# Optimization experiments

Measured on AMD Instinct MI355X. Metric: run time of the kernel, lower is better.

The kernel has to match this reference:

```python
import jax, jax.numpy as jnp
import numpy as np

N, IN_DIM, OUT_DIM = 8192, 256, 64
NEG_INF = -9e15
SLOPE = 0.2


def setup_inputs() -> dict:
    key = jax.random.key(0)
    k1, k2, k3, k4 = jax.random.split(key, 4)
    h = jax.random.normal(k1, (N, IN_DIM), dtype=jnp.float32)
    adj = jax.random.randint(k2, (N, N), 0, 2, dtype=jnp.int32)
    W = jax.random.normal(k3, (IN_DIM, OUT_DIM), dtype=jnp.float32) * (1.0 / np.sqrt(IN_DIM))
    a = jax.random.normal(k4, (2 * OUT_DIM,), dtype=jnp.float32) * (1.0 / np.sqrt(2 * OUT_DIM))
    return {"h": h, "adj": adj, "W": W, "a": a}


def reference(h, adj, W, a):
    # Wh: [N, F]
    Wh = h @ W
    F = Wh.shape[-1]
    # a([Wh_i ; Wh_j]) decomposes: score_ij = a_left.Wh_i + a_right.Wh_j
    f_i = Wh @ a[:F]          # [N]
    f_j = Wh @ a[F:]          # [N]
    e = f_i[:, None] + f_j[None, :]            # [N, N] broadcast sum
    e = jnp.where(e >= 0, e, SLOPE * e)         # leaky relu (0.2)
    e = jnp.where(adj > 0, e, jnp.float32(NEG_INF))
    alpha = jax.nn.softmax(e, axis=1)           # row softmax over neighbors j
    return alpha @ Wh                            # [N, F]
```

## Files before the change

### kernel.cpp

```cpp
#include <hip/hip_runtime.h>

#define NN 8192
#define KDIM 256
#define FDIM 64
#define SLOPEC 0.2f

typedef __attribute__((ext_vector_type(8))) short bf16x8;
typedef __attribute__((ext_vector_type(4))) float f32x4;

__device__ __forceinline__ unsigned short f2bf(float x) {
    union { float f; unsigned u; } v; v.f = x;
    unsigned r = v.u + 0x7FFFu + ((v.u >> 16) & 1u);
    return (unsigned short)(r >> 16);
}

__device__ __forceinline__ float wred64(float v) {
    v += __shfl_xor(v, 1);
    v += __shfl_xor(v, 2);
    v += __shfl_xor(v, 4);
    v += __shfl_xor(v, 8);
    v += __shfl_xor(v, 16);
    v += __shfl_xor(v, 32);
    return v;
}

__global__ __launch_bounds__(256) void gat_phase1(
    const float* __restrict__ h, const float* __restrict__ W,
    const float* __restrict__ a, unsigned short* __restrict__ wfrag,
    float* __restrict__ fi, float* __restrict__ fj)
{
    __shared__ unsigned short wht_s[FDIM][20];
    const int tid = threadIdx.x;
    const int f  = tid & 63;
    const int rg = tid >> 6;
    const int i0 = blockIdx.x << 4;

    const float* __restrict__ h0 = h + (size_t)(i0 + rg * 4) * KDIM;
    const float* __restrict__ h1 = h0 + KDIM;
    const float* __restrict__ h2 = h0 + 2 * KDIM;
    const float* __restrict__ h3 = h0 + 3 * KDIM;

    float acc0 = 0.f, acc1 = 0.f, acc2 = 0.f, acc3 = 0.f;
    #pragma unroll 4
    for (int k4 = 0; k4 < KDIM / 4; ++k4) {
        const float4 r0 = *(const float4*)(h0 + k4 * 4);
        const float4 r1 = *(const float4*)(h1 + k4 * 4);
        const float4 r2 = *(const float4*)(h2 + k4 * 4);
        const float4 r3 = *(const float4*)(h3 + k4 * 4);
        const float w0 = W[(k4 * 4 + 0) * FDIM + f];
        const float w1 = W[(k4 * 4 + 1) * FDIM + f];
        const float w2 = W[(k4 * 4 + 2) * FDIM + f];
        const float w3 = W[(k4 * 4 + 3) * FDIM + f];
        acc0 += r0.x * w0 + r0.y * w1 + r0.z * w2 + r0.w * w3;
        acc1 += r1.x * w0 + r1.y * w1 + r1.z * w2 + r1.w * w3;
        acc2 += r2.x * w0 + r2.y * w1 + r2.z * w2 + r2.w * w3;
        acc3 += r3.x * w0 + r3.y * w1 + r3.z * w2 + r3.w * w3;
    }

    const int r0i = rg * 4;
    wht_s[f][r0i + 0] = f2bf(acc0);
    wht_s[f][r0i + 1] = f2bf(acc1);
    wht_s[f][r0i + 2] = f2bf(acc2);
    wht_s[f][r0i + 3] = f2bf(acc3);

    const float aL = a[f];
    const float aR = a[FDIM + f];
    float s;
    s = wred64(acc0 * aL); if (f == 0) fi[i0 + r0i + 0] = s;
    s = wred64(acc1 * aL); if (f == 0) fi[i0 + r0i + 1] = s;
    s = wred64(acc2 * aL); if (f == 0) fi[i0 + r0i + 2] = s;
    s = wred64(acc3 * aL); if (f == 0) fi[i0 + r0i + 3] = s;
    s = wred64(acc0 * aR); if (f == 0) fj[i0 + r0i + 0] = s;
    s = wred64(acc1 * aR); if (f == 0) fj[i0 + r0i + 1] = s;
    s = wred64(acc2 * aR); if (f == 0) fj[i0 + r0i + 2] = s;
    s = wred64(acc3 * aR); if (f == 0) fj[i0 + r0i + 3] = s;

    __syncthreads();
    if (tid < 128) {
        const int li2 = tid & 15;
        const int q2  = (tid >> 4) & 1;
        const int b   = tid >> 5;
        const int t   = i0 >> 5;
        const int hh  = (i0 >> 4) & 1;
        const int feat = b * 16 + li2;
        const ushort4 lo = *(const ushort4*)&wht_s[feat][q2 * 8];
        const ushort4 hi = *(const ushort4*)&wht_s[feat][q2 * 8 + 4];
        const int lg = (hh * 2 + q2) * 16 + li2;
        unsigned short* dst = wfrag + (size_t)t * 2048 + b * 512 + lg * 8;
        *(ushort4*)(dst)     = lo;
        *(ushort4*)(dst + 4) = hi;
    }
}

__global__ __launch_bounds__(256) void gat_adjmask(
    const int* __restrict__ adj, unsigned* __restrict__ mask)
{
    const int tid = threadIdx.x;
    const int l  = tid & 63;
    const int gw = (blockIdx.x << 2) | (tid >> 6);
    const int* __restrict__ row = adj + (size_t)gw * NN;
    unsigned* __restrict__ mrow = mask + (size_t)gw * (NN / 32);

    const int wsel = (l & 7) * 4;
    #pragma unroll 1
    for (int base = 0; base < 32; base += 8) {
        int4 v[8];
        #pragma unroll
        for (int k = 0; k < 8; ++k)
            v[k] = *(const int4*)(row + (base + k) * 256 + l * 4);
        #pragma unroll
        for (int k = 0; k < 8; ++k) {
            unsigned nib = (unsigned)(v[k].x > 0) | ((unsigned)(v[k].y > 0) << 1)
                         | ((unsigned)(v[k].z > 0) << 2) | ((unsigned)(v[k].w > 0) << 3);
            unsigned part = nib << wsel;
            part |= __shfl_xor(part, 1);
            part |= __shfl_xor(part, 2);
            part |= __shfl_xor(part, 4);
            if ((l & 7) == 0) mrow[(base + k) * 8 + (l >> 3)] = part;
        }
    }
}

__global__ __launch_bounds__(512, 4) void gat_phase2(
    const unsigned* __restrict__ mask, const unsigned short* __restrict__ wfrag,
    const float* __restrict__ fi, const float* __restrict__ fjg,
    float* __restrict__ out)
{
    __shared__ float fj_s[NN];
    __shared__ float zred[128];

    const int tid = threadIdx.x;
    const int w  = tid >> 6;
    const int l  = tid & 63;
    const int li = l & 15;
    const int q  = l >> 4;
    const int qo = q * 8;
    const int i0 = blockIdx.x << 4;

    for (int t4 = tid; t4 < NN / 4; t4 += 512)
        ((float4*)fj_s)[t4] = ((const float4*)fjg)[t4];
    __syncthreads();

    const float f_i = fi[i0 + li];
    const unsigned* __restrict__ mrow = mask + (size_t)(i0 + li) * (NN / 32);
    const unsigned short* __restrict__ wf = wfrag + l * 8;

    f32x4 acc0 = {0.f, 0.f, 0.f, 0.f};
    f32x4 acc1 = {0.f, 0.f, 0.f, 0.f};
    f32x4 acc2 = {0.f, 0.f, 0.f, 0.f};
    f32x4 acc3 = {0.f, 0.f, 0.f, 0.f};
    float z = 0.f;

    #pragma unroll 4
    for (int tw = w; tw < NN / 32; tw += 8) {
        const int jg = tw * 32 + qo;
        const unsigned mq = mrow[tw] >> qo;
        const float4 fj0 = *(const float4*)(fj_s + jg);
        const float4 fj1 = *(const float4*)(fj_s + jg + 4);
        const unsigned short* wt = wf + (size_t)tw * 2048;
        const bf16x8 b0 = *(const bf16x8*)(wt);
        const bf16x8 b1 = *(const bf16x8*)(wt + 512);
        const bf16x8 b2 = *(const bf16x8*)(wt + 1024);
        const bf16x8 b3 = *(const bf16x8*)(wt + 1536);
        float e0 = f_i + fj0.x; e0 = fmaxf(e0, SLOPEC * e0);
        float e1 = f_i + fj0.y; e1 = fmaxf(e1, SLOPEC * e1);
        float e2 = f_i + fj0.z; e2 = fmaxf(e2, SLOPEC * e2);
        float e3 = f_i + fj0.w; e3 = fmaxf(e3, SLOPEC * e3);
        float e4 = f_i + fj1.x; e4 = fmaxf(e4, SLOPEC * e4);
        float e5 = f_i + fj1.y; e5 = fmaxf(e5, SLOPEC * e5);
        float e6 = f_i + fj1.z; e6 = fmaxf(e6, SLOPEC * e6);
        float e7 = f_i + fj1.w; e7 = fmaxf(e7, SLOPEC * e7);
        const float p0 = (mq &   1u) ? __expf(e0) : 0.f;
        const float p1 = (mq &   2u) ? __expf(e1) : 0.f;
        const float p2 = (mq &   4u) ? __expf(e2) : 0.f;
        const float p3 = (mq &   8u) ? __expf(e3) : 0.f;
        const float p4 = (mq &  16u) ? __expf(e4) : 0.f;
        const float p5 = (mq &  32u) ? __expf(e5) : 0.f;
        const float p6 = (mq &  64u) ? __expf(e6) : 0.f;
        const float p7 = (mq & 128u) ? __expf(e7) : 0.f;
        z += ((p0 + p1) + (p2 + p3)) + ((p4 + p5) + (p6 + p7));
        bf16x8 afrag;
        afrag[0] = (short)f2bf(p0);
        afrag[1] = (short)f2bf(p1);
        afrag[2] = (short)f2bf(p2);
        afrag[3] = (short)f2bf(p3);
        afrag[4] = (short)f2bf(p4);
        afrag[5] = (short)f2bf(p5);
        afrag[6] = (short)f2bf(p6);
        afrag[7] = (short)f2bf(p7);
        acc0 = __builtin_amdgcn_mfma_f32_16x16x32_bf16(afrag, b0, acc0, 0, 0, 0);
        acc1 = __builtin_amdgcn_mfma_f32_16x16x32_bf16(afrag, b1, acc1, 0, 0, 0);
        acc2 = __builtin_amdgcn_mfma_f32_16x16x32_bf16(afrag, b2, acc2, 0, 0, 0);
        acc3 = __builtin_amdgcn_mfma_f32_16x16x32_bf16(afrag, b3, acc3, 0, 0, 0);
    }

    __syncthreads();
    float* red = fj_s;
    #pragma unroll
    for (int r = 0; r < 4; ++r) {
        red[(w * 16 + q * 4 + r) * 64 + 0 * 16 + li] = acc0[r];
        red[(w * 16 + q * 4 + r) * 64 + 1 * 16 + li] = acc1[r];
        red[(w * 16 + q * 4 + r) * 64 + 2 * 16 + li] = acc2[r];
        red[(w * 16 + q * 4 + r) * 64 + 3 * 16 + li] = acc3[r];
    }
    z += __shfl_xor(z, 16);
    z += __shfl_xor(z, 32);
    if (q == 0) zred[w * 16 + li] = z;
    __syncthreads();

    const int f  = tid & 63;
    const int ig = tid >> 6;
    #pragma unroll
    for (int cc = 0; cc < 2; ++cc) {
        const int i = cc * 8 + ig;
        const float v = ((red[(0 * 16 + i) * 64 + f] + red[(1 * 16 + i) * 64 + f])
                       + (red[(2 * 16 + i) * 64 + f] + red[(3 * 16 + i) * 64 + f]))
                      + ((red[(4 * 16 + i) * 64 + f] + red[(5 * 16 + i) * 64 + f])
                       + (red[(6 * 16 + i) * 64 + f] + red[(7 * 16 + i) * 64 + f]));
        const float zz = ((zred[0 * 16 + i] + zred[1 * 16 + i]) + (zred[2 * 16 + i] + zred[3 * 16 + i]))
                       + ((zred[4 * 16 + i] + zred[5 * 16 + i]) + (zred[6 * 16 + i] + zred[7 * 16 + i]));
        out[(size_t)(i0 + i) * FDIM + f] = v / zz;
    }
}

extern "C" void kernel_launch(void* const* d_in, const int* in_sizes, int n_in,
                              void* d_out, int out_size, void* d_ws, size_t ws_size,
                              hipStream_t stream) {
    const float* h   = (const float*)d_in[0];
    const int*   adj = (const int*)d_in[1];
    const float* W   = (const float*)d_in[2];
    const float* a   = (const float*)d_in[3];
    float* out = (float*)d_out;

    unsigned short* wfrag = (unsigned short*)d_ws;
    float* fi = (float*)((char*)d_ws + (size_t)NN * FDIM * 2);
    float* fj = fi + NN;
    unsigned* mask = (unsigned*)((char*)d_ws + (2u << 20));

    gat_phase1<<<NN / 16, 256, 0, stream>>>(h, W, a, wfrag, fi, fj);
    gat_adjmask<<<NN / 4, 256, 0, stream>>>(adj, mask);
    gat_phase2<<<NN / 16, 512, 0, stream>>>(mask, wfrag, fi, fj, out);
}
```

Baseline: 107.2 us.

## Factor exp of leaky-relu into packed fp16 products and use byte masks

The softmax numerator exp(leaky(fi+fj)) is rewritten as max(exp(fi)exp(fj), exp(.2fi)exp(.2fj)), with the per-column exponentials precomputed in fp16 shared memory. This replaces per-element transcendental work with packed f16 multiply/max. The adjacency mask becomes a byte-per-entry 0xFF mask applied by AND, and the row sum is taken by an extra MFMA against ones. The trade-offs: the mask grows to 64MB of extra traffic instead of a bitmask, and fp16 overflow or precision loss is possible in the exponent products. The weights also move from bf16 to fp16.

```diff
diff --git a/kernel.cpp b/kernel.cpp
--- a/kernel.cpp
+++ b/kernel.cpp
@@ -1,17 +1,23 @@
 #include <hip/hip_runtime.h>
+#include <hip/hip_fp16.h>
 
 #define NN 8192
 #define KDIM 256
 #define FDIM 64
-#define SLOPEC 0.2f
-
-typedef __attribute__((ext_vector_type(8))) short bf16x8;
+
+typedef __attribute__((ext_vector_type(8))) _Float16 f16x8;
 typedef __attribute__((ext_vector_type(4))) float f32x4;
 
-__device__ __forceinline__ unsigned short f2bf(float x) {
-    union { float f; unsigned u; } v; v.f = x;
-    unsigned r = v.u + 0x7FFFu + ((v.u >> 16) & 1u);
-    return (unsigned short)(r >> 16);
+union H2U { __half2 h; unsigned u; };
+union HU  { __half h; unsigned short u; };
+
+__device__ __forceinline__ unsigned h2u(__half2 h) { H2U x; x.h = h; return x.u; }
+
+__device__ __forceinline__ unsigned pkmul(unsigned a, unsigned b) {
+    unsigned d; asm("v_pk_mul_f16 %0, %1, %2" : "=v"(d) : "v"(a), "v"(b)); return d;
+}
+__device__ __forceinline__ unsigned pkmax(unsigned a, unsigned b) {
+    unsigned d; asm("v_pk_max_f16 %0, %1, %2" : "=v"(d) : "v"(a), "v"(b)); return d;
 }
 
 __device__ __forceinline__ float wred64(float v) {
@@ -57,11 +63,15 @@
         acc3 += r3.x * w0 + r3.y * w1 + r3.z * w2 + r3.w * w3;
     }
 
+    HU c0; c0.h = __float2half(acc0);
+    HU c1; c1.h = __float2half(acc1);
+    HU c2; c2.h = __float2half(acc2);
+    HU c3; c3.h = __float2half(acc3);
     const int r0i = rg * 4;
-    wht_s[f][r0i + 0] = f2bf(acc0);
-    wht_s[f][r0i + 1] = f2bf(acc1);
-    wht_s[f][r0i + 2] = f2bf(acc2);
-    wht_s[f][r0i + 3] = f2bf(acc3);
+    wht_s[f][r0i + 0] = c0.u;
+    wht_s[f][r0i + 1] = c1.u;
+    wht_s[f][r0i + 2] = c2.u;
+    wht_s[f][r0i + 3] = c3.u;
 
     const float aL = a[f];
     const float aR = a[FDIM + f];
@@ -93,40 +103,33 @@
 }
 
 __global__ __launch_bounds__(256) void gat_adjmask(
-    const int* __restrict__ adj, unsigned* __restrict__ mask)
+    const int4* __restrict__ adj4, unsigned* __restrict__ bm32)
 {
-    const int tid = threadIdx.x;
-    const int l  = tid & 63;
-    const int gw = (blockIdx.x << 2) | (tid >> 6);
-    const int* __restrict__ row = adj + (size_t)gw * NN;
-    unsigned* __restrict__ mrow = mask + (size_t)gw * (NN / 32);
-
-    const int wsel = (l & 7) * 4;
+    const int gtid = (blockIdx.x << 8) | threadIdx.x;
+    const int TOT = 2048 * 256;
     #pragma unroll 1
-    for (int base = 0; base < 32; base += 8) {
+    for (int s0 = 0; s0 < 32; s0 += 8) {
         int4 v[8];
         #pragma unroll
         for (int k = 0; k < 8; ++k)
-            v[k] = *(const int4*)(row + (base + k) * 256 + l * 4);
+            v[k] = adj4[(size_t)(s0 + k) * TOT + gtid];
         #pragma unroll
         for (int k = 0; k < 8; ++k) {
-            unsigned nib = (unsigned)(v[k].x > 0) | ((unsigned)(v[k].y > 0) << 1)
-                         | ((unsigned)(v[k].z > 0) << 2) | ((unsigned)(v[k].w > 0) << 3);
-            unsigned part = nib << wsel;
-            part |= __shfl_xor(part, 1);
-            part |= __shfl_xor(part, 2);
-            part |= __shfl_xor(part, 4);
-            if ((l & 7) == 0) mrow[(base + k) * 8 + (l >> 3)] = part;
+            const unsigned b = (v[k].x > 0 ? 0x000000FFu : 0u)
+                             | (v[k].y > 0 ? 0x0000FF00u : 0u)
+                             | (v[k].z > 0 ? 0x00FF0000u : 0u)
+                             | (v[k].w > 0 ? 0xFF000000u : 0u);
+            bm32[(size_t)(s0 + k) * TOT + gtid] = b;
         }
     }
 }
 
 __global__ __launch_bounds__(512, 4) void gat_phase2(
-    const unsigned* __restrict__ mask, const unsigned short* __restrict__ wfrag,
+    const unsigned char* __restrict__ bm, const unsigned short* __restrict__ wfrag,
     const float* __restrict__ fi, const float* __restrict__ fjg,
     float* __restrict__ out)
 {
-    __shared__ float fj_s[NN];
+    __shared__ unsigned Ebuf[NN];
     __shared__ float zred[128];
 
     const int tid = threadIdx.x;
@@ -137,65 +140,62 @@
     const int qo = q * 8;
     const int i0 = blockIdx.x << 4;
 
-    for (int t4 = tid; t4 < NN / 4; t4 += 512)
-        ((float4*)fj_s)[t4] = ((const float4*)fjg)[t4];
-    __syncthreads();
-
-    const float f_i = fi[i0 + li];
-    const unsigned* __restrict__ mrow = mask + (size_t)(i0 + li) * (NN / 32);
-    const unsigned short* __restrict__ wf = wfrag + l * 8;
+    unsigned* E1p = Ebuf;
+    unsigned* E2p = Ebuf + NN / 2;
+    for (int t = tid; t < NN / 2; t += 512) {
+        const float2 f2 = ((const float2*)fjg)[t];
+        E1p[t] = h2u(__floats2half2_rn(__expf(f2.x), __expf(f2.y)));
+        E2p[t] = h2u(__floats2half2_rn(__expf(0.2f * f2.x), __expf(0.2f * f2.y)));
+    }
+    __syncthreads();
+
+    const float fiv = fi[i0 + li];
+    const unsigned e1i2 = h2u(__floats2half2_rn(__expf(fiv), __expf(fiv)));
+    const unsigned e2i2 = h2u(__floats2half2_rn(__expf(0.2f * fiv), __expf(0.2f * fiv)));
+
+    const unsigned char*  __restrict__ brow = bm + (size_t)(i0 + li) * NN;
+    const unsigned short* __restrict__ wf   = wfrag + l * 8;
 
     f32x4 acc0 = {0.f, 0.f, 0.f, 0.f};
     f32x4 acc1 = {0.f, 0.f, 0.f, 0.f};
     f32x4 acc2 = {0.f, 0.f, 0.f, 0.f};
     f32x4 acc3 = {0.f, 0.f, 0.f, 0.f};
-    float z = 0.f;
+    f32x4 accz = {0.f, 0.f, 0.f, 0.f};
+    const f16x8 ones = { (_Float16)1.f, (_Float16)1.f, (_Float16)1.f, (_Float16)1.f,
+                         (_Float16)1.f, (_Float16)1.f, (_Float16)1.f, (_Float16)1.f };
 
     #pragma unroll 4
     for (int tw = w; tw < NN / 32; tw += 8) {
         const int jg = tw * 32 + qo;
-        const unsigned mq = mrow[tw] >> qo;
-        const float4 fj0 = *(const float4*)(fj_s + jg);
-        const float4 fj1 = *(const float4*)(fj_s + jg + 4);
+        const uint2 mw  = *(const uint2*)(brow + jg);
+        const uint4 e1w = *(const uint4*)(E1p + (jg >> 1));
+        const uint4 e2w = *(const uint4*)(E2p + (jg >> 1));
         const unsigned short* wt = wf + (size_t)tw * 2048;
-        const bf16x8 b0 = *(const bf16x8*)(wt);
-        const bf16x8 b1 = *(const bf16x8*)(wt + 512);
-        const bf16x8 b2 = *(const bf16x8*)(wt + 1024);
-        const bf16x8 b3 = *(const bf16x8*)(wt + 1536);
-        float e0 = f_i + fj0.x; e0 = fmaxf(e0, SLOPEC * e0);
-        float e1 = f_i + fj0.y; e1 = fmaxf(e1, SLOPEC * e1);
-        float e2 = f_i + fj0.z; e2 = fmaxf(e2, SLOPEC * e2);
-        float e3 = f_i + fj0.w; e3 = fmaxf(e3, SLOPEC * e3);
-        float e4 = f_i + fj1.x; e4 = fmaxf(e4, SLOPEC * e4);
-        float e5 = f_i + fj1.y; e5 = fmaxf(e5, SLOPEC * e5);
-        float e6 = f_i + fj1.z; e6 = fmaxf(e6, SLOPEC * e6);
-        float e7 = f_i + fj1.w; e7 = fmaxf(e7, SLOPEC * e7);
-        const float p0 = (mq &   1u) ? __expf(e0) : 0.f;
-        const float p1 = (mq &   2u) ? __expf(e1) : 0.f;
-        const float p2 = (mq &   4u) ? __expf(e2) : 0.f;
-        const float p3 = (mq &   8u) ? __expf(e3) : 0.f;
-        const float p4 = (mq &  16u) ? __expf(e4) : 0.f;
-        const float p5 = (mq &  32u) ? __expf(e5) : 0.f;
-        const float p6 = (mq &  64u) ? __expf(e6) : 0.f;
-        const float p7 = (mq & 128u) ? __expf(e7) : 0.f;
-        z += ((p0 + p1) + (p2 + p3)) + ((p4 + p5) + (p6 + p7));
-        bf16x8 afrag;
-        afrag[0] = (short)f2bf(p0);
-        afrag[1] = (short)f2bf(p1);
-        afrag[2] = (short)f2bf(p2);
-        afrag[3] = (short)f2bf(p3);
-        afrag[4] = (short)f2bf(p4);
-        afrag[5] = (short)f2bf(p5);
-        afrag[6] = (short)f2bf(p6);
-        afrag[7] = (short)f2bf(p7);
-        acc0 = __builtin_amdgcn_mfma_f32_16x16x32_bf16(afrag, b0, acc0, 0, 0, 0);
-        acc1 = __builtin_amdgcn_mfma_f32_16x16x32_bf16(afrag, b1, acc1, 0, 0, 0);
-        acc2 = __builtin_amdgcn_mfma_f32_16x16x32_bf16(afrag, b2, acc2, 0, 0, 0);
-        acc3 = __builtin_amdgcn_mfma_f32_16x16x32_bf16(afrag, b3, acc3, 0, 0, 0);
-    }
-
-    __syncthreads();
-    float* red = fj_s;
+        const f16x8 b0 = *(const f16x8*)(wt);
+        const f16x8 b1 = *(const f16x8*)(wt + 512);
+        const f16x8 b2 = *(const f16x8*)(wt + 1024);
+        const f16x8 b3 = *(const f16x8*)(wt + 1536);
+
+        const unsigned mm0 = __builtin_amdgcn_perm(0u, mw.x, 0x01010000u);
+        const unsigned mm1 = __builtin_amdgcn_perm(0u, mw.x, 0x03030202u);
+        const unsigned mm2 = __builtin_amdgcn_perm(0u, mw.y, 0x01010000u);
+        const unsigned mm3 = __builtin_amdgcn_perm(0u, mw.y, 0x03030202u);
+
+        union { unsigned u[4]; f16x8 v; } af;
+        af.u[0] = pkmax(pkmul(e1i2, e1w.x), pkmul(e2i2, e2w.x)) & mm0;
+        af.u[1] = pkmax(pkmul(e1i2, e1w.y), pkmul(e2i2, e2w.y)) & mm1;
+        af.u[2] = pkmax(pkmul(e1i2, e1w.z), pkmul(e2i2, e2w.z)) & mm2;
+        af.u[3] = pkmax(pkmul(e1i2, e1w.w), pkmul(e2i2, e2w.w)) & mm3;
+
+        acc0 = __builtin_amdgcn_mfma_f32_16x16x32_f16(af.v, b0, acc0, 0, 0, 0);
+        acc1 = __builtin_amdgcn_mfma_f32_16x16x32_f16(af.v, b1, acc1, 0, 0, 0);
+        acc2 = __builtin_amdgcn_mfma_f32_16x16x32_f16(af.v, b2, acc2, 0, 0, 0);
+        acc3 = __builtin_amdgcn_mfma_f32_16x16x32_f16(af.v, b3, acc3, 0, 0, 0);
+        accz = __builtin_amdgcn_mfma_f32_16x16x32_f16(af.v, ones, accz, 0, 0, 0);
+    }
+
+    __syncthreads();
+    float* red = (float*)Ebuf;
     #pragma unroll
     for (int r = 0; r < 4; ++r) {
         red[(w * 16 + q * 4 + r) * 64 + 0 * 16 + li] = acc0[r];
@@ -203,9 +203,11 @@
         red[(w * 16 + q * 4 + r) * 64 + 2 * 16 + li] = acc2[r];
         red[(w * 16 + q * 4 + r) * 64 + 3 * 16 + li] = acc3[r];
     }
-    z += __shfl_xor(z, 16);
-    z += __shfl_xor(z, 32);
-    if (q == 0) zred[w * 16 + li] = z;
+    if (li == 0) {
+        #pragma unroll
+        for (int r = 0; r < 4; ++r)
+            zred[w * 16 + q * 4 + r] = accz[r];
+    }
     __syncthreads();
 
     const int f  = tid & 63;
@@ -235,9 +237,9 @@
     unsigned short* wfrag = (unsigned short*)d_ws;
     float* fi = (float*)((char*)d_ws + (size_t)NN * FDIM * 2);
     float* fj = fi + NN;
-    unsigned* mask = (unsigned*)((char*)d_ws + (2u << 20));
+    unsigned char* bm = (unsigned char*)d_ws + (2u << 20);
 
     gat_phase1<<<NN / 16, 256, 0, stream>>>(h, W, a, wfrag, fi, fj);
-    gat_adjmask<<<NN / 4, 256, 0, stream>>>(adj, mask);
-    gat_phase2<<<NN / 16, 512, 0, stream>>>(mask, wfrag, fi, fj, out);
-}
+    gat_adjmask<<<2048, 256, 0, stream>>>((const int4*)adj, (unsigned*)bm);
+    gat_phase2<<<NN / 16, 512, 0, stream>>>(bm, wfrag, fi, fj, out);
+}
```

Result: slower. 130.2 us (+21.4%).
